# Kernel tuning notes

Hardware: AMD Instinct MI355X
Metric: run time of the kernel (lower is better)

Reference implementation:

```python
import jax, jax.numpy as jnp
import numpy as np

EPS = 1e-6
NUM_HEADS = 8
HEAD_DIM = 64


def _elu_plus_one(x):
    # ELU(x) + 1 : positive feature map used for linear attention
    return jax.nn.elu(x) + 1.0


def setup_inputs() -> dict:
    key = jax.random.key(0)
    ks = jax.random.split(key, 10)
    B, S, D = 1, 4096, 512  # batch, seq_len, hidden_size
    P = NUM_HEADS * HEAD_DIM  # proj_dim == hidden_size here
    scale = 0.05  # keep projections numerically tame
    return {
        "hidden_states": jax.random.normal(ks[0], (B, S, D), jnp.float32),
        "Wq": jax.random.normal(ks[1], (D, P), jnp.float32) * scale,
        "bq": jnp.zeros((P,), jnp.float32),
        "Wk": jax.random.normal(ks[2], (D, P), jnp.float32) * scale,
        "bk": jnp.zeros((P,), jnp.float32),
        "Wv": jax.random.normal(ks[3], (D, P), jnp.float32) * scale,
        "bv": jnp.zeros((P,), jnp.float32),
        "Wo": jax.random.normal(ks[4], (P, D), jnp.float32) * scale,
        # persistent per-head tensor-product memory: M [H, Dh, Dh], z [H, Dh]
        "M_mem": jax.random.uniform(ks[5], (NUM_HEADS, HEAD_DIM, HEAD_DIM), jnp.float32),
        "z_mem": jax.random.uniform(ks[6], (NUM_HEADS, HEAD_DIM), jnp.float32),
    }


def reference(hidden_states, Wq, bq, Wk, bk, Wv, bv, Wo, M_mem, z_mem):
    B, S, D = hidden_states.shape
    H, Dh = NUM_HEADS, HEAD_DIM

    def split_heads(t):
        # [B, S, H*Dh] -> [B, H, S, Dh]
        return t.reshape(B, S, H, Dh).transpose(0, 2, 1, 3)

    q = split_heads(hidden_states @ Wq + bq)
    k = split_heads(hidden_states @ Wk + bk)
    v = split_heads(hidden_states @ Wv + bv)

    sq = _elu_plus_one(q)  # sigma(Q)  [B,H,S,Dh]
    sk = _elu_plus_one(k)  # sigma(K)  [B,H,S,Dh]

    # kv[t] = sigma(k_t) (x) v_t ; causal prefix sums, seeded by persistent memory
    kv = sk[..., :, None] * v[..., None, :]            # [B,H,S,Dh,Dh]
    cumsum_kv = jnp.cumsum(kv, axis=2) + M_mem[None, :, None]  # + M per head
    cumsum_k = jnp.cumsum(sk, axis=2) + z_mem[None, :, None]   # + z per head

    numerator = jnp.einsum('bhsd,bhsde->bhse', sq, cumsum_kv)  # [B,H,S,Dh]
    denominator = jnp.einsum('bhsd,bhsd->bhs', sq, cumsum_k)   # [B,H,S]
    out = numerator / (denominator[..., None] + EPS)

    out = out.transpose(0, 2, 1, 3).reshape(B, S, H * Dh)  # merge heads
    return out @ Wo
```

## Files before the change

### kernel.cpp

```cpp
#include <hip/hip_runtime.h>
#include <hip/hip_bf16.h>
#include <math.h>

#define S_LEN 4096
#define D_HID 512
#define P_DIM 512
#define H_NUM 8
#define DH 64
#define NC 64
#define EPS 1e-6f

typedef __attribute__((ext_vector_type(8))) short short8;
typedef __attribute__((ext_vector_type(4))) float f32x4;
typedef __attribute__((ext_vector_type(4))) unsigned short ushort4v;

static __device__ __forceinline__ float b2f(unsigned short u) {
  return __builtin_bit_cast(float, ((unsigned int)u) << 16);
}
static __device__ __forceinline__ unsigned short f2b(float f) {
  unsigned int u = __builtin_bit_cast(unsigned int, f);
  u = (u + 0x7fff + ((u >> 16) & 1)) >> 16;
  return (unsigned short)u;
}
static __device__ __forceinline__ int swz(int row, int d) {
  return d ^ ((row & 7) << 3);
}

#define GLOAD_LDS16(g, l)                                              \
  __builtin_amdgcn_global_load_lds(                                    \
      (const __attribute__((address_space(1))) unsigned int*)(g),      \
      (__attribute__((address_space(3))) unsigned int*)(l), 16, 0, 0)

__global__ __launch_bounds__(256) void convert_hs(
    const float4* __restrict__ in, unsigned short* __restrict__ out, int n4) {
  int idx = blockIdx.x * 256 + threadIdx.x;
  if (idx < n4) {
    float4 v = in[idx];
    ushort4v o = {f2b(v.x), f2b(v.y), f2b(v.z), f2b(v.w)};
    *(ushort4v*)(out + (size_t)idx * 4) = o;
  }
}

__global__ __launch_bounds__(256) void transpose_w(
    const float* __restrict__ Wq, const float* __restrict__ Wk,
    const float* __restrict__ Wv, const float* __restrict__ Wo,
    unsigned short* __restrict__ WT) {
  __shared__ float t[32][33];
  int z = blockIdx.z;
  const float* src = (z == 0) ? Wq : (z == 1) ? Wk : (z == 2) ? Wv : Wo;
  int bx = blockIdx.x * 32;
  int by = blockIdx.y * 32;
  int lx = threadIdx.x & 31, ly = threadIdx.x >> 5;
#pragma unroll
  for (int i = 0; i < 4; i++)
    t[ly + i * 8][lx] = src[(size_t)(by + ly + i * 8) * 512 + bx + lx];
  __syncthreads();
#pragma unroll
  for (int i = 0; i < 4; i++) {
    int n = bx + ly + i * 8;
    WT[((size_t)z * 512 + n) * 512 + by + lx] = f2b(t[lx][ly + i * 8]);
  }
}

template <int MODE>
__global__ __launch_bounds__(256) void mfma_gemm(
    const unsigned short* __restrict__ A, const unsigned short* __restrict__ BT,
    const float* __restrict__ bq, const float* __restrict__ bk,
    const float* __restrict__ bv, unsigned short* __restrict__ sqz,
    unsigned short* __restrict__ skz, unsigned short* __restrict__ skTz,
    unsigned short* __restrict__ vTz, float* __restrict__ outf) {
  __shared__ unsigned short As[128 * 32];
  __shared__ unsigned short Bs[128 * 32];
  int tid = threadIdx.x;
  int w = tid >> 6, lane = tid & 63;
  int bm = blockIdx.x * 128, bn = blockIdx.y * 128;
  f32x4 acc[4][4] = {};

  int ldrow = lane >> 2;
  int ldk = (lane & 3) * 8;

  for (int k0 = 0; k0 < 512; k0 += 32) {
#pragma unroll
    for (int i = 0; i < 2; i++) {
      int seg = i * 4 + w;
      int row = seg * 16 + ldrow;
      GLOAD_LDS16(A + (size_t)(bm + row) * 512 + k0 + ldk, As + seg * 512);
      GLOAD_LDS16(BT + (size_t)(bn + row) * 512 + k0 + ldk, Bs + seg * 512);
    }
    __syncthreads();

    int wr = w >> 1, wc = w & 1;
    short8 a[4], b[4];
#pragma unroll
    for (int m = 0; m < 4; m++) {
      int arow = wr * 64 + m * 16 + (lane & 15);
      a[m] = *(const short8*)(As + arow * 32 + (lane >> 4) * 8);
    }
#pragma unroll
    for (int n = 0; n < 4; n++) {
      int brow = wc * 64 + n * 16 + (lane & 15);
      b[n] = *(const short8*)(Bs + brow * 32 + (lane >> 4) * 8);
    }
#pragma unroll
    for (int m = 0; m < 4; m++)
#pragma unroll
      for (int n = 0; n < 4; n++)
        acc[m][n] = __builtin_amdgcn_mfma_f32_16x16x32_bf16(a[m], b[n],
                                                            acc[m][n], 0, 0, 0);
    __syncthreads();
  }

  int wr = w >> 1, wc = w & 1;
#pragma unroll
  for (int m = 0; m < 4; m++) {
    int r0 = bm + wr * 64 + m * 16 + ((lane >> 4) << 2);
#pragma unroll
    for (int n = 0; n < 4; n++) {
      int col = bn + wc * 64 + n * 16 + (lane & 15);
      if (MODE == 0) {
        int m512 = col & 511, hh = m512 >> 6, dd = m512 & 63;
        float bias = (col < 512) ? bq[m512] : (col < 1024 ? bk[m512] : bv[m512]);
#pragma unroll
        for (int j = 0; j < 4; j++) {
          int s = r0 + j;
          float val = acc[m][n][j] + bias;
          if (col < 1024) val = (val > 0.f) ? (val + 1.f) : __expf(val);
          unsigned short bb = f2b(val);
          size_t tpos = ((size_t)hh * 64 + dd) * S_LEN + (s & ~63) +
                        ((s & 63) ^ ((dd & 7) << 3));
          if (col < 512) {
            sqz[((size_t)hh * S_LEN + s) * 64 + swz(s, dd)] = bb;
          } else if (col < 1024) {
            skz[((size_t)hh * S_LEN + s) * 64 + swz(s, dd)] = bb;
            skTz[tpos] = bb;
          } else {
            vTz[tpos] = bb;
          }
        }
      } else {
#pragma unroll
        for (int j = 0; j < 4; j++)
          outf[(size_t)(r0 + j) * 512 + col] = acc[m][n][j];
      }
    }
  }
}

__global__ __launch_bounds__(256) void chunk_sum_mfma(
    const unsigned short* __restrict__ vTz, const unsigned short* __restrict__ skTz,
    float* __restrict__ KVt, float* __restrict__ ksum) {
  __shared__ unsigned short vt_lds[64 * 64];
  __shared__ unsigned short skt_lds[64 * 64];
  int h = blockIdx.x / NC, c = blockIdx.x % NC;
  int tid = threadIdx.x, w = tid >> 6, lane = tid & 63;
  int lr = lane >> 3, lc = (lane & 7) * 8;
#pragma unroll
  for (int i = 0; i < 2; i++) {
    int seg = w * 2 + i;
    GLOAD_LDS16(vTz + ((size_t)h * 64 + seg * 8 + lr) * S_LEN + c * 64 + lc,
                vt_lds + seg * 512);
    GLOAD_LDS16(skTz + ((size_t)h * 64 + seg * 8 + lr) * S_LEN + c * 64 + lc,
                skt_lds + seg * 512);
  }
  __syncthreads();

  int fr = lane & 15, kg = (lane >> 4) * 8;
  short8 onesA = {};
  if (fr == 0) {
#pragma unroll
    for (int j = 0; j < 8; j++) onesA[j] = (short)0x3F80;
  }
  f32x4 acc[4] = {};
  f32x4 accK[4] = {};
#pragma unroll
  for (int k0 = 0; k0 < 64; k0 += 32) {
    int e = w * 16 + fr;
    short8 a = *(const short8*)(vt_lds + e * 64 + ((k0 + kg) ^ ((e & 7) << 3)));
    short8 b[4];
#pragma unroll
    for (int nt = 0; nt < 4; nt++) {
      int d = nt * 16 + fr;
      b[nt] = *(const short8*)(skt_lds + d * 64 + ((k0 + kg) ^ ((d & 7) << 3)));
    }
#pragma unroll
    for (int nt = 0; nt < 4; nt++)
      acc[nt] = __builtin_amdgcn_mfma_f32_16x16x32_bf16(a, b[nt], acc[nt], 0, 0, 0);
    if (w == 0) {
#pragma unroll
      for (int nt = 0; nt < 4; nt++)
        accK[nt] =
            __builtin_amdgcn_mfma_f32_16x16x32_bf16(onesA, b[nt], accK[nt], 0, 0, 0);
    }
  }
  int e0 = w * 16 + (lane >> 4) * 4;
  size_t base = (size_t)(h * NC + c) * 4096;
#pragma unroll
  for (int nt = 0; nt < 4; nt++)
#pragma unroll
    for (int j = 0; j < 4; j++)
      KVt[base + (size_t)(e0 + j) * 64 + nt * 16 + fr] = acc[nt][j];
  if (w == 0 && lane < 16) {
#pragma unroll
    for (int nt = 0; nt < 4; nt++)
      ksum[(size_t)(h * NC + c) * 64 + nt * 16 + lane] = accK[nt][0];
  }
}

__global__ __launch_bounds__(256) void prefix_kernel(
    const float* __restrict__ KVt, const float* __restrict__ ksum,
    const float* __restrict__ M_mem, const float* __restrict__ z_mem,
    unsigned short* __restrict__ KVpz, unsigned short* __restrict__ zp_bf) {
  int h = blockIdx.x >> 4, g = blockIdx.x & 15;
  int tid = threadIdx.x;
  int entry = g * 256 + tid, e = entry >> 6, d = entry & 63;
  float pref = M_mem[h * 4096 + d * 64 + e];
  size_t i0 = (size_t)(h * NC) * 4096 + (size_t)e * 64 + d;
  size_t o0 = (size_t)(h * NC) * 4096 + (size_t)e * 64 + swz(e, d);
  for (int c = 0; c < NC; c += 4) {
    float v0 = KVt[i0 + (size_t)c * 4096];
    float v1 = KVt[i0 + (size_t)(c + 1) * 4096];
    float v2 = KVt[i0 + (size_t)(c + 2) * 4096];
    float v3 = KVt[i0 + (size_t)(c + 3) * 4096];
    KVpz[o0 + (size_t)c * 4096] = f2b(pref);
    pref += v0;
    KVpz[o0 + (size_t)(c + 1) * 4096] = f2b(pref);
    pref += v1;
    KVpz[o0 + (size_t)(c + 2) * 4096] = f2b(pref);
    pref += v2;
    KVpz[o0 + (size_t)(c + 3) * 4096] = f2b(pref);
    pref += v3;
  }
  if (g == 0 && tid < 64) {
    float zp = z_mem[h * 64 + tid];
    for (int c = 0; c < NC; c += 4) {
      float u0 = ksum[(size_t)(h * NC + c) * 64 + tid];
      float u1 = ksum[(size_t)(h * NC + c + 1) * 64 + tid];
      float u2 = ksum[(size_t)(h * NC + c + 2) * 64 + tid];
      float u3 = ksum[(size_t)(h * NC + c + 3) * 64 + tid];
      zp_bf[(size_t)(h * NC + c) * 64 + tid] = f2b(zp);
      zp += u0;
      zp_bf[(size_t)(h * NC + c + 1) * 64 + tid] = f2b(zp);
      zp += u1;
      zp_bf[(size_t)(h * NC + c + 2) * 64 + tid] = f2b(zp);
      zp += u2;
      zp_bf[(size_t)(h * NC + c + 3) * 64 + tid] = f2b(zp);
      zp += u3;
    }
  }
}

__global__ __launch_bounds__(256) void attn_mfma(
    const unsigned short* __restrict__ sqz, const unsigned short* __restrict__ skz,
    const unsigned short* __restrict__ vTz, const unsigned short* __restrict__ KVpz,
    const unsigned short* __restrict__ zp_bf, unsigned short* __restrict__ attnb) {
  __shared__ unsigned short sq_lds[4096], sk_lds[4096];
  __shared__ unsigned short btv_lds[80 * 64], btm_lds[80 * 64];
  __shared__ unsigned short shi_lds[4096], slo_lds[4096];
  int h = blockIdx.x / NC, c = blockIdx.x % NC;
  int tid = threadIdx.x, w = tid >> 6, lane = tid & 63;

  {
    const unsigned short* sq_g = sqz + ((size_t)h * S_LEN + c * 64) * 64;
    const unsigned short* sk_g = skz + ((size_t)h * S_LEN + c * 64) * 64;
    const unsigned short* km_g = KVpz + (size_t)(h * NC + c) * 4096;
    int lr = lane >> 3, lc = (lane & 7) * 8;
#pragma unroll
    for (int i = 0; i < 2; i++) {
      int seg = w * 2 + i;
      GLOAD_LDS16(sq_g + seg * 512 + lane * 8, sq_lds + seg * 512);
      GLOAD_LDS16(sk_g + seg * 512 + lane * 8, sk_lds + seg * 512);
      GLOAD_LDS16(km_g + seg * 512 + lane * 8, btm_lds + seg * 512);
      GLOAD_LDS16(vTz + ((size_t)h * 64 + seg * 8 + lr) * S_LEN + c * 64 + lc,
                  btv_lds + seg * 512);
    }
  }
  if (tid < 8) {
    short8 one;
#pragma unroll
    for (int j = 0; j < 8; j++) one[j] = (short)0x3F80;
    *(short8*)(btv_lds + 64 * 64 + tid * 8) = one;
    *(short8*)(btm_lds + 64 * 64 + tid * 8) =
        *(const short8*)(zp_bf + (size_t)(h * NC + c) * 64 + tid * 8);
  }
  __syncthreads();

  int fr = lane & 15, kg8 = (lane >> 4) * 8;
  int ta = w * 16 + fr;
  int sw_a = (ta & 7) << 3;

  f32x4 accS[4] = {};
#pragma unroll
  for (int k0 = 0; k0 < 64; k0 += 32) {
    short8 a = *(const short8*)(sq_lds + ta * 64 + ((k0 + kg8) ^ sw_a));
#pragma unroll
    for (int nt = 0; nt < 4; nt++) {
      int tp = nt * 16 + fr;
      short8 b = *(const short8*)(sk_lds + tp * 64 + ((k0 + kg8) ^ ((tp & 7) << 3)));
      accS[nt] = __builtin_amdgcn_mfma_f32_16x16x32_bf16(a, b, accS[nt], 0, 0, 0);
    }
  }
  int r0 = (lane >> 4) * 4;
#pragma unroll
  for (int nt = 0; nt < 4; nt++) {
    int tp = nt * 16 + fr;
#pragma unroll
    for (int j = 0; j < 4; j++) {
      int t = w * 16 + r0 + j;
      float s = (tp <= t) ? accS[nt][j] : 0.f;
      unsigned short hi = f2b(s);
      unsigned short lo = f2b(s - b2f(hi));
      shi_lds[t * 64 + swz(t, tp)] = hi;
      slo_lds[t * 64 + swz(t, tp)] = lo;
    }
  }
  f32x4 acc2[5] = {};
#pragma unroll
  for (int ks = 0; ks < 6; ks++) {
    const unsigned short* asrc = (ks < 2) ? shi_lds : (ks < 4) ? slo_lds : sq_lds;
    const unsigned short* bsrc = (ks < 4) ? btv_lds : btm_lds;
    int ak = (ks & 1) * 32 + kg8;
    short8 a = *(const short8*)(asrc + ta * 64 + (ak ^ sw_a));
#pragma unroll
    for (int nt = 0; nt < 5; nt++) {
      int n = nt * 16 + fr;
      short8 b = *(const short8*)(bsrc + n * 64 + (ak ^ ((n & 7) << 3)));
      acc2[nt] = __builtin_amdgcn_mfma_f32_16x16x32_bf16(a, b, acc2[nt], 0, 0, 0);
    }
  }
  float inv[4];
#pragma unroll
  for (int j = 0; j < 4; j++) {
    float dj = __shfl(acc2[4][j], (lane & 48), 64);
    inv[j] = 1.f / (dj + EPS);
  }
  int srow = c * 64 + w * 16 + r0;
#pragma unroll
  for (int nt = 0; nt < 4; nt++) {
    int col = h * 64 + nt * 16 + fr;
#pragma unroll
    for (int j = 0; j < 4; j++)
      attnb[(size_t)(srow + j) * 512 + col] = f2b(acc2[nt][j] * inv[j]);
  }
}

extern "C" void kernel_launch(void* const* d_in, const int* in_sizes, int n_in,
                              void* d_out, int out_size, void* d_ws,
                              size_t ws_size, hipStream_t stream) {
  const float* hs = (const float*)d_in[0];
  const float* Wq = (const float*)d_in[1];
  const float* bq = (const float*)d_in[2];
  const float* Wk = (const float*)d_in[3];
  const float* bk = (const float*)d_in[4];
  const float* Wv = (const float*)d_in[5];
  const float* bv = (const float*)d_in[6];
  const float* Wo = (const float*)d_in[7];
  const float* M_mem = (const float*)d_in[8];
  const float* z_mem = (const float*)d_in[9];
  float* out = (float*)d_out;

  unsigned short* hs_bf = (unsigned short*)d_ws;
  unsigned short* WT = hs_bf + (size_t)S_LEN * D_HID;
  unsigned short* sqz = WT + (size_t)4 * 512 * 512;
  unsigned short* skz = sqz + (size_t)H_NUM * S_LEN * DH;
  unsigned short* skTz = skz + (size_t)H_NUM * S_LEN * DH;
  unsigned short* vTz = skTz + (size_t)H_NUM * S_LEN * DH;
  unsigned short* attnb = vTz + (size_t)H_NUM * S_LEN * DH;
  unsigned short* KVpz = attnb + (size_t)S_LEN * P_DIM;
  unsigned short* zp_bf = KVpz + (size_t)H_NUM * NC * DH * DH;
  float* KVt = (float*)(zp_bf + (size_t)H_NUM * NC * DH);
  float* ksum = KVt + (size_t)H_NUM * NC * DH * DH;

  convert_hs<<<2048, 256, 0, stream>>>((const float4*)hs, hs_bf,
                                       S_LEN * D_HID / 4);
  dim3 tg(16, 16, 4);
  transpose_w<<<tg, 256, 0, stream>>>(Wq, Wk, Wv, Wo, WT);

  dim3 pg(S_LEN / 128, 1536 / 128);
  mfma_gemm<0><<<pg, 256, 0, stream>>>(hs_bf, WT, bq, bk, bv, sqz, skz, skTz,
                                       vTz, nullptr);

  chunk_sum_mfma<<<H_NUM * NC, 256, 0, stream>>>(vTz, skTz, KVt, ksum);
  prefix_kernel<<<H_NUM * 16, 256, 0, stream>>>(KVt, ksum, M_mem, z_mem, KVpz,
                                                zp_bf);
  attn_mfma<<<H_NUM * NC, 256, 0, stream>>>(sqz, skz, vTz, KVpz, zp_bf, attnb);

  dim3 og(S_LEN / 128, 512 / 128);
  mfma_gemm<1><<<og, 256, 0, stream>>>(attnb, WT + (size_t)3 * 512 * 512,
                                       nullptr, nullptr, nullptr, nullptr,
                                       nullptr, nullptr, nullptr, out);
}
```

Baseline: 136.0 us.

## Merge prep kernels, shrink GEMM M-tile, stage transposed epilogue through LDS

Fuses the hidden-state conversion and weight transpose into a single prep launch to save one kernel launch. The GEMM M-tile drops from 128 to 64 rows, doubling the block count so more CUs stay busy on the small output GEMM. The QKV epilogue now writes the transposed sk and v tiles into a swizzled LDS buffer that is unioned with the operand tiles. It then stores them as coalesced 16-byte rows instead of scattered 2-byte global writes, at the cost of an extra barrier and lower per-block reuse.

```diff
diff --git a/kernel.cpp b/kernel.cpp
--- a/kernel.cpp
+++ b/kernel.cpp
@@ -31,34 +31,34 @@
       (const __attribute__((address_space(1))) unsigned int*)(g),      \
       (__attribute__((address_space(3))) unsigned int*)(l), 16, 0, 0)
 
-__global__ __launch_bounds__(256) void convert_hs(
-    const float4* __restrict__ in, unsigned short* __restrict__ out, int n4) {
-  int idx = blockIdx.x * 256 + threadIdx.x;
-  if (idx < n4) {
-    float4 v = in[idx];
-    ushort4v o = {f2b(v.x), f2b(v.y), f2b(v.z), f2b(v.w)};
-    *(ushort4v*)(out + (size_t)idx * 4) = o;
-  }
-}
-
-__global__ __launch_bounds__(256) void transpose_w(
-    const float* __restrict__ Wq, const float* __restrict__ Wk,
-    const float* __restrict__ Wv, const float* __restrict__ Wo,
+__global__ __launch_bounds__(256) void prep_kernel(
+    const float* __restrict__ hs, const float* __restrict__ Wq,
+    const float* __restrict__ Wk, const float* __restrict__ Wv,
+    const float* __restrict__ Wo, unsigned short* __restrict__ hs_bf,
     unsigned short* __restrict__ WT) {
   __shared__ float t[32][33];
-  int z = blockIdx.z;
-  const float* src = (z == 0) ? Wq : (z == 1) ? Wk : (z == 2) ? Wv : Wo;
-  int bx = blockIdx.x * 32;
-  int by = blockIdx.y * 32;
-  int lx = threadIdx.x & 31, ly = threadIdx.x >> 5;
-#pragma unroll
-  for (int i = 0; i < 4; i++)
-    t[ly + i * 8][lx] = src[(size_t)(by + ly + i * 8) * 512 + bx + lx];
-  __syncthreads();
-#pragma unroll
-  for (int i = 0; i < 4; i++) {
-    int n = bx + ly + i * 8;
-    WT[((size_t)z * 512 + n) * 512 + by + lx] = f2b(t[lx][ly + i * 8]);
+  int bid = blockIdx.x, tid = threadIdx.x;
+  if (bid < 2048) {
+    int idx = bid * 256 + tid;
+    float4 v = ((const float4*)hs)[idx];
+    ushort4v o = {f2b(v.x), f2b(v.y), f2b(v.z), f2b(v.w)};
+    *(ushort4v*)(hs_bf + (size_t)idx * 4) = o;
+  } else {
+    int b2 = bid - 2048;
+    int z = b2 >> 8, r = b2 & 255;
+    const float* src = (z == 0) ? Wq : (z == 1) ? Wk : (z == 2) ? Wv : Wo;
+    int bx = (r & 15) * 32;
+    int by = (r >> 4) * 32;
+    int lx = tid & 31, ly = tid >> 5;
+#pragma unroll
+    for (int i = 0; i < 4; i++)
+      t[ly + i * 8][lx] = src[(size_t)(by + ly + i * 8) * 512 + bx + lx];
+    __syncthreads();
+#pragma unroll
+    for (int i = 0; i < 4; i++) {
+      int n = bx + ly + i * 8;
+      WT[((size_t)z * 512 + n) * 512 + by + lx] = f2b(t[lx][ly + i * 8]);
+    }
   }
 }
 
@@ -69,40 +69,42 @@
     const float* __restrict__ bv, unsigned short* __restrict__ sqz,
     unsigned short* __restrict__ skz, unsigned short* __restrict__ skTz,
     unsigned short* __restrict__ vTz, float* __restrict__ outf) {
-  __shared__ unsigned short As[128 * 32];
-  __shared__ unsigned short Bs[128 * 32];
+  union SU {
+    struct {
+      unsigned short As[64 * 32];
+      unsigned short Bs[128 * 32];
+    } st;
+    unsigned short epsT[128 * 72];
+  };
+  __shared__ SU sh;
   int tid = threadIdx.x;
   int w = tid >> 6, lane = tid & 63;
-  int bm = blockIdx.x * 128, bn = blockIdx.y * 128;
-  f32x4 acc[4][4] = {};
+  int bm = blockIdx.x * 64, bn = blockIdx.y * 128;
+  f32x4 acc[2][4] = {};
 
   int ldrow = lane >> 2;
   int ldk = (lane & 3) * 8;
+  int wr = w >> 1, wc = w & 1;
+  int fr = lane & 15, kg8 = (lane >> 4) * 8, q4 = (lane >> 4) * 4;
 
   for (int k0 = 0; k0 < 512; k0 += 32) {
-#pragma unroll
-    for (int i = 0; i < 2; i++) {
-      int seg = i * 4 + w;
-      int row = seg * 16 + ldrow;
-      GLOAD_LDS16(A + (size_t)(bm + row) * 512 + k0 + ldk, As + seg * 512);
-      GLOAD_LDS16(BT + (size_t)(bn + row) * 512 + k0 + ldk, Bs + seg * 512);
-    }
+    GLOAD_LDS16(A + (size_t)(bm + w * 16 + ldrow) * 512 + k0 + ldk,
+                sh.st.As + w * 512);
+    GLOAD_LDS16(BT + (size_t)(bn + w * 16 + ldrow) * 512 + k0 + ldk,
+                sh.st.Bs + w * 512);
+    GLOAD_LDS16(BT + (size_t)(bn + (w + 4) * 16 + ldrow) * 512 + k0 + ldk,
+                sh.st.Bs + (w + 4) * 512);
     __syncthreads();
 
-    int wr = w >> 1, wc = w & 1;
-    short8 a[4], b[4];
-#pragma unroll
-    for (int m = 0; m < 4; m++) {
-      int arow = wr * 64 + m * 16 + (lane & 15);
-      a[m] = *(const short8*)(As + arow * 32 + (lane >> 4) * 8);
-    }
-#pragma unroll
-    for (int n = 0; n < 4; n++) {
-      int brow = wc * 64 + n * 16 + (lane & 15);
-      b[n] = *(const short8*)(Bs + brow * 32 + (lane >> 4) * 8);
-    }
-#pragma unroll
-    for (int m = 0; m < 4; m++)
+    short8 a[2], b[4];
+#pragma unroll
+    for (int m = 0; m < 2; m++)
+      a[m] = *(const short8*)(sh.st.As + (wr * 32 + m * 16 + fr) * 32 + kg8);
+#pragma unroll
+    for (int n = 0; n < 4; n++)
+      b[n] = *(const short8*)(sh.st.Bs + (wc * 64 + n * 16 + fr) * 32 + kg8);
+#pragma unroll
+    for (int m = 0; m < 2; m++)
 #pragma unroll
       for (int n = 0; n < 4; n++)
         acc[m][n] = __builtin_amdgcn_mfma_f32_16x16x32_bf16(a[m], b[n],
@@ -110,37 +112,61 @@
     __syncthreads();
   }
 
-  int wr = w >> 1, wc = w & 1;
-#pragma unroll
-  for (int m = 0; m < 4; m++) {
-    int r0 = bm + wr * 64 + m * 16 + ((lane >> 4) << 2);
-#pragma unroll
-    for (int n = 0; n < 4; n++) {
-      int col = bn + wc * 64 + n * 16 + (lane & 15);
-      if (MODE == 0) {
-        int m512 = col & 511, hh = m512 >> 6, dd = m512 & 63;
-        float bias = (col < 512) ? bq[m512] : (col < 1024 ? bk[m512] : bv[m512]);
+  if (MODE == 0) {
+    int region = bn >> 9;
+    int hh_base = (bn & 511) >> 6;
+#pragma unroll
+    for (int m = 0; m < 2; m++) {
+      int sl0 = wr * 32 + m * 16 + q4;
+#pragma unroll
+      for (int n = 0; n < 4; n++) {
+        int cl = wc * 64 + n * 16 + fr;
+        int col = bn + cl;
+        int m512 = col & 511;
+        int hh = m512 >> 6, dd = m512 & 63;
+        float bias = (region == 0) ? bq[m512]
+                     : (region == 1) ? bk[m512] : bv[m512];
 #pragma unroll
         for (int j = 0; j < 4; j++) {
-          int s = r0 + j;
+          int sl = sl0 + j;
+          int s = bm + sl;
           float val = acc[m][n][j] + bias;
-          if (col < 1024) val = (val > 0.f) ? (val + 1.f) : __expf(val);
+          if (region < 2) val = (val > 0.f) ? (val + 1.f) : __expf(val);
           unsigned short bb = f2b(val);
-          size_t tpos = ((size_t)hh * 64 + dd) * S_LEN + (s & ~63) +
-                        ((s & 63) ^ ((dd & 7) << 3));
-          if (col < 512) {
+          if (region == 0) {
             sqz[((size_t)hh * S_LEN + s) * 64 + swz(s, dd)] = bb;
-          } else if (col < 1024) {
+          } else if (region == 1) {
             skz[((size_t)hh * S_LEN + s) * 64 + swz(s, dd)] = bb;
-            skTz[tpos] = bb;
+            sh.epsT[cl * 72 + (sl ^ ((cl & 7) << 3))] = bb;
           } else {
-            vTz[tpos] = bb;
+            sh.epsT[cl * 72 + (sl ^ ((cl & 7) << 3))] = bb;
           }
         }
-      } else {
+      }
+    }
+    __syncthreads();
+    if (region >= 1) {
+      unsigned short* Tdst = (region == 1) ? skTz : vTz;
+#pragma unroll
+      for (int i = 0; i < 4; i++) {
+        int G = tid + 256 * i;
+        int gq = G & 7;
+        int cl = G >> 3;
+        int hh = hh_base + (cl >> 6), dd = cl & 63;
+        short8 v8 = *(const short8*)(sh.epsT + cl * 72 + gq * 8);
+        *(short8*)(Tdst + ((size_t)(hh * 64 + dd)) * S_LEN + bm + gq * 8) = v8;
+      }
+    }
+  } else {
+#pragma unroll
+    for (int m = 0; m < 2; m++) {
+      int sl0 = wr * 32 + m * 16 + q4;
+#pragma unroll
+      for (int n = 0; n < 4; n++) {
+        int col = bn + wc * 64 + n * 16 + fr;
 #pragma unroll
         for (int j = 0; j < 4; j++)
-          outf[(size_t)(r0 + j) * 512 + col] = acc[m][n][j];
+          outf[(size_t)(bm + sl0 + j) * 512 + col] = acc[m][n][j];
       }
     }
   }
@@ -370,12 +396,9 @@
   float* KVt = (float*)(zp_bf + (size_t)H_NUM * NC * DH);
   float* ksum = KVt + (size_t)H_NUM * NC * DH * DH;
 
-  convert_hs<<<2048, 256, 0, stream>>>((const float4*)hs, hs_bf,
-                                       S_LEN * D_HID / 4);
-  dim3 tg(16, 16, 4);
-  transpose_w<<<tg, 256, 0, stream>>>(Wq, Wk, Wv, Wo, WT);
-
-  dim3 pg(S_LEN / 128, 1536 / 128);
+  prep_kernel<<<3072, 256, 0, stream>>>(hs, Wq, Wk, Wv, Wo, hs_bf, WT);
+
+  dim3 pg(S_LEN / 64, 1536 / 128);
   mfma_gemm<0><<<pg, 256, 0, stream>>>(hs_bf, WT, bq, bk, bv, sqz, skz, skTz,
                                        vTz, nullptr);
 
@@ -384,7 +407,7 @@
                                                 zp_bf);
   attn_mfma<<<H_NUM * NC, 256, 0, stream>>>(sqz, skz, vTz, KVpz, zp_bf, attnb);
 
-  dim3 og(S_LEN / 128, 512 / 128);
+  dim3 og(S_LEN / 64, 512 / 128);
   mfma_gemm<1><<<og, 256, 0, stream>>>(attnb, WT + (size_t)3 * 512 * 512,
                                        nullptr, nullptr, nullptr, nullptr,
                                        nullptr, nullptr, nullptr, out);
```

Result: faster. 126.1 us (-7.3%).
